# Kernel optimization log

Hardware: AMD Instinct MI355X
Metric: run time of the kernel (lower is better)

Reference implementation:

```python
import jax, jax.numpy as jnp
import numpy as np

DROPOUT_P = 0.5


def normalize_adj(A):
    # A_tilda = A + I ; A_hat = D^-0.5 A_tilda D^-0.5
    # The torch code does this with diag_embed + two bmm (O(N^3));
    # mathematically it is row/col broadcasting (O(N^2)).
    B, N, _ = A.shape
    A_tilda = A + jnp.eye(N, dtype=A.dtype)
    d_inv_sqrt = jnp.sum(A_tilda, axis=2) ** -0.5          # [B, N]
    return d_inv_sqrt[:, :, None] * A_tilda * d_inv_sqrt[:, None, :]


def gcn_layer(X, A_hat, W, b):
    # standard Kipf GCN layer: A_hat @ (X @ W) + b
    return jnp.einsum('bnm,bmd->bnd', A_hat, X @ W) + b


def setup_inputs() -> dict:
    key = jax.random.key(0)
    ks = jax.random.split(key, 6)
    B, N, Din, H, C = 8, 2048, 64, 64, 16
    X = jax.random.normal(ks[0], (B, N, Din), dtype=jnp.float32)
    A = jax.random.uniform(ks[1], (B, N, N), dtype=jnp.float32)
    W1 = jax.random.normal(ks[2], (Din, H), dtype=jnp.float32) * (1.0 / np.sqrt(Din))
    b1 = jax.random.normal(ks[3], (H,), dtype=jnp.float32) * 0.01
    W2 = jax.random.normal(ks[4], (H, C), dtype=jnp.float32) * (1.0 / np.sqrt(H))
    b2 = jax.random.normal(ks[5], (C,), dtype=jnp.float32) * 0.01
    return {"X": X, "A": A, "W1": W1, "b1": b1, "W2": W2, "b2": b2}


def reference(X, A, W1, b1, W2, b2):
    A_hat = normalize_adj(A)
    h = jax.nn.relu(gcn_layer(X, A_hat, W1, b1))
    # F.dropout default training=True -> apply dropout with a fixed key
    keep = jax.random.bernoulli(jax.random.key(42), 1.0 - DROPOUT_P, h.shape)
    h = jnp.where(keep, h / (1.0 - DROPOUT_P), 0.0).astype(h.dtype)
    return gcn_layer(h, A_hat, W2, b2)
```

## Files before the change

### kernel.cpp

```cpp
#include <hip/hip_runtime.h>

#define BN 16384
#define NN 2048
#define DD 64
#define CC 16

typedef short bf16x8 __attribute__((ext_vector_type(8)));
typedef float f32x4 __attribute__((ext_vector_type(4)));
typedef unsigned short u16x4 __attribute__((ext_vector_type(4)));

__device__ __forceinline__ f32x4 mfma16(bf16x8 a, bf16x8 b, f32x4 c) {
  return __builtin_amdgcn_mfma_f32_16x16x32_bf16(a, b, c, 0, 0, 0);
}
__device__ __forceinline__ unsigned short f2bf(float f) {
  unsigned u = __float_as_uint(f);
  return (unsigned short)((u + 0x7FFFu + ((u >> 16) & 1u)) >> 16);
}
__device__ __forceinline__ float bf2f(unsigned short h) {
  return __uint_as_float(((unsigned)h) << 16);
}

__device__ __forceinline__ unsigned tf_bits(unsigned i) {
  unsigned x0 = 0u;
  unsigned x1 = i;
  const unsigned k0 = 0u, k1 = 42u, k2 = 0x1BD11BDAu ^ 0u ^ 42u;
  x0 += k0; x1 += k1;
#define TFR(r) { x0 += x1; x1 = (x1 << (r)) | (x1 >> (32 - (r))); x1 ^= x0; }
  TFR(13) TFR(15) TFR(26) TFR(6)
  x0 += k1; x1 += k2 + 1u;
  TFR(17) TFR(29) TFR(16) TFR(24)
  x0 += k2; x1 += k0 + 2u;
  TFR(13) TFR(15) TFR(26) TFR(6)
  x0 += k0; x1 += k1 + 3u;
  TFR(17) TFR(29) TFR(16) TFR(24)
  x0 += k1; x1 += k2 + 4u;
  TFR(13) TFR(15) TFR(26) TFR(6)
  x0 += k2; x1 += k0 + 5u;
#undef TFR
  return x0 ^ x1;
}


__global__ __launch_bounds__(256) void k_deg(const float* __restrict__ A,
    float* __restrict__ dis, unsigned short* __restrict__ Abf)
{
  const int w = threadIdx.x >> 6, lane = threadIdx.x & 63;
  const size_t row = (size_t)blockIdx.x * 4 + w;
  const float4* Arow = (const float4*)(A + row * NN);
  unsigned short* Brow = Abf + row * NN;
  float s = 0.f;
#pragma unroll
  for (int it = 0; it < 8; ++it) {
    float4 v = Arow[lane + 64 * it];
    s += (v.x + v.y) + (v.z + v.w);
    u16x4 p = { f2bf(v.x), f2bf(v.y), f2bf(v.z), f2bf(v.w) };
    *(u16x4*)(Brow + lane * 4 + it * 256) = p;
  }
#pragma unroll
  for (int m = 32; m; m >>= 1) s += __shfl_xor(s, m, 64);
  if (lane == 0) dis[row] = 1.0f / sqrtf(s + 1.0f);
}

__global__ __launch_bounds__(256) void k_xw1(const float* __restrict__ X,
    const float* __restrict__ W1, const float* __restrict__ dis,
    unsigned short* __restrict__ Y1s, unsigned short* __restrict__ Y1sT)
{
  __shared__ float Xs[64 * 65];
  const int tid = threadIdx.x;
  const int r0 = blockIdx.x * 64;
  const int b = r0 >> 11, kr0 = r0 & (NN - 1);
#pragma unroll
  for (int it = 0; it < 16; ++it) {
    int idx = it * 256 + tid;
    Xs[(idx >> 6) * 65 + (idx & 63)] = X[(size_t)r0 * DD + idx];
  }
  __syncthreads();
  const int wq = __builtin_amdgcn_readfirstlane(tid >> 6);
  const int lane = tid & 63;
  const int row = r0 + lane;
  float acc[16];
#pragma unroll
  for (int c = 0; c < 16; ++c) acc[c] = 0.f;
  const float* Xr = Xs + lane * 65;
  const float* W1p = W1 + wq * 16;
#pragma unroll
  for (int k = 0; k < 64; ++k) {
    const float xv = Xr[k];
#pragma unroll
    for (int c = 0; c < 16; ++c) acc[c] += xv * W1p[k * DD + c];
  }
  const float dv = dis[row];
#pragma unroll
  for (int c = 0; c < 16; ++c) acc[c] *= dv;
#pragma unroll
  for (int q = 0; q < 4; ++q) {
    u16x4 p = { f2bf(acc[q*4]), f2bf(acc[q*4+1]), f2bf(acc[q*4+2]), f2bf(acc[q*4+3]) };
    *(u16x4*)(Y1s + (size_t)row * DD + wq * 16 + q * 4) = p;
  }
#pragma unroll
  for (int it = 0; it < 16; ++it)
    Y1sT[((size_t)b * DD + wq * 16 + it) * NN + kr0 + lane] = f2bf(acc[it]);
}

__global__ __launch_bounds__(256) void k_gemm1(const unsigned short* __restrict__ Abf,
    const unsigned short* __restrict__ Y1sT, float* __restrict__ Z1)
{
  const int Mb = blockIdx.x >> 2, ks = blockIdx.x & 3;
  const int w = __builtin_amdgcn_readfirstlane((int)threadIdx.x >> 6);
  const int lane = threadIdx.x & 63;
  const int m15 = lane & 15, quad = lane >> 4;
  const int b = Mb >> 4;
  const int k0 = ks * 512 + quad * 8;
  const unsigned short* Ap0 = Abf + ((size_t)Mb * 128 + w * 16 + m15) * NN + k0;
  const unsigned short* Ap1 = Ap0 + (size_t)64 * NN;
  const unsigned short* Bp  = Y1sT + ((size_t)b * DD + m15) * NN + k0;
  const f32x4 zero = 0.f;
  f32x4 acc[2][4];
#pragma unroll
  for (int m = 0; m < 2; ++m)
#pragma unroll
    for (int t = 0; t < 4; ++t) acc[m][t] = zero;
  bf16x8 a0 = *(const bf16x8*)Ap0;
  bf16x8 a1 = *(const bf16x8*)Ap1;
  bf16x8 b0 = *(const bf16x8*)(Bp);
  bf16x8 b1 = *(const bf16x8*)(Bp + 16 * NN);
  bf16x8 b2 = *(const bf16x8*)(Bp + 32 * NN);
  bf16x8 b3 = *(const bf16x8*)(Bp + 48 * NN);
  for (int kk = 0; kk < 16; ++kk) {
    const int off = (kk < 15) ? (kk + 1) * 32 : 0;
    bf16x8 na0 = *(const bf16x8*)(Ap0 + off);
    bf16x8 na1 = *(const bf16x8*)(Ap1 + off);
    bf16x8 nb0 = *(const bf16x8*)(Bp + off);
    bf16x8 nb1 = *(const bf16x8*)(Bp + 16 * NN + off);
    bf16x8 nb2 = *(const bf16x8*)(Bp + 32 * NN + off);
    bf16x8 nb3 = *(const bf16x8*)(Bp + 48 * NN + off);
    acc[0][0] = mfma16(a0, b0, acc[0][0]);
    acc[0][1] = mfma16(a0, b1, acc[0][1]);
    acc[0][2] = mfma16(a0, b2, acc[0][2]);
    acc[0][3] = mfma16(a0, b3, acc[0][3]);
    acc[1][0] = mfma16(a1, b0, acc[1][0]);
    acc[1][1] = mfma16(a1, b1, acc[1][1]);
    acc[1][2] = mfma16(a1, b2, acc[1][2]);
    acc[1][3] = mfma16(a1, b3, acc[1][3]);
    a0 = na0; a1 = na1; b0 = nb0; b1 = nb1; b2 = nb2; b3 = nb3;
  }
  const int rb0 = Mb * 128 + w * 16 + quad * 4;
#pragma unroll
  for (int m = 0; m < 2; ++m)
#pragma unroll
    for (int t = 0; t < 4; ++t)
#pragma unroll
      for (int r = 0; r < 4; ++r)
        Z1[((size_t)ks * BN + rb0 + m * 64 + r) * DD + t * 16 + m15] = acc[m][t][r];
}

__global__ __launch_bounds__(256) void k_epi1(const float* __restrict__ Z1,
    const unsigned short* __restrict__ Y1s, const float* __restrict__ dis,
    const float* __restrict__ b1, const float* __restrict__ W2,
    unsigned short* __restrict__ Y2sT)
{
  __shared__ float hs[64 * 65];
  __shared__ float W2l[DD * CC];
  const int tid = threadIdx.x;
  const int r0 = blockIdx.x * 64;
  const int b = r0 >> 11, kr0 = r0 & (NN - 1);
  *(float4*)(W2l + tid * 4) = *(const float4*)(W2 + tid * 4);
  const int n = tid & 63, wg = tid >> 6;
  const float bias = b1[n];
#pragma unroll
  for (int i = 0; i < 16; ++i) {
    const int rl = wg * 16 + i;
    const size_t row = (size_t)r0 + rl;
    const size_t o = row * DD + n;
    float z = bf2f(Y1s[o]);
#pragma unroll
    for (int p = 0; p < 4; ++p) z += Z1[((size_t)p * BN + row) * DD + n];
    float h = fmaxf(dis[row] * z + bias, 0.f);
    const unsigned bits = tf_bits((unsigned)o);
    h = (bits >> 31) ? 0.f : (h + h);
    hs[rl * 65 + n] = h;
  }
  __syncthreads();
  const int c = tid & 15, rg = tid >> 4;
  float y[4];
#pragma unroll
  for (int rr = 0; rr < 4; ++rr) {
    const int rl = rg * 4 + rr;
    float s = 0.f;
#pragma unroll
    for (int k = 0; k < 64; ++k) s += hs[rl * 65 + k] * W2l[k * CC + c];
    y[rr] = dis[r0 + rl] * s;
  }
  u16x4 pk = { f2bf(y[0]), f2bf(y[1]), f2bf(y[2]), f2bf(y[3]) };
  *(u16x4*)(Y2sT + ((size_t)b * CC + c) * NN + kr0 + rg * 4) = pk;
}

__global__ __launch_bounds__(256) void k_gemm2(const unsigned short* __restrict__ Abf,
    const unsigned short* __restrict__ Y2sT, float* __restrict__ Z2)
{
  const int Mb = blockIdx.x >> 3, ks = blockIdx.x & 7;
  const int w = __builtin_amdgcn_readfirstlane((int)threadIdx.x >> 6);
  const int lane = threadIdx.x & 63;
  const int m15 = lane & 15, quad = lane >> 4;
  const int b = Mb >> 3;
  const int k0 = ks * 256 + quad * 8;
  const unsigned short* Ap = Abf + ((size_t)Mb * 256 + w * 16 + m15) * NN + k0;
  const unsigned short* Bp = Y2sT + ((size_t)b * CC + m15) * NN + k0;
  const f32x4 zero = 0.f;
  f32x4 acc[4];
#pragma unroll
  for (int m = 0; m < 4; ++m) acc[m] = zero;
  bf16x8 a[4];
#pragma unroll
  for (int m = 0; m < 4; ++m) a[m] = *(const bf16x8*)(Ap + (size_t)m * 64 * NN);
  bf16x8 bb = *(const bf16x8*)Bp;
  for (int kk = 0; kk < 8; ++kk) {
    const int off = (kk < 7) ? (kk + 1) * 32 : 0;
    bf16x8 na[4];
#pragma unroll
    for (int m = 0; m < 4; ++m) na[m] = *(const bf16x8*)(Ap + (size_t)m * 64 * NN + off);
    bf16x8 nbb = *(const bf16x8*)(Bp + off);
#pragma unroll
    for (int m = 0; m < 4; ++m) acc[m] = mfma16(a[m], bb, acc[m]);
#pragma unroll
    for (int m = 0; m < 4; ++m) a[m] = na[m];
    bb = nbb;
  }
  const int rb0 = Mb * 256 + w * 16 + quad * 4;
#pragma unroll
  for (int m = 0; m < 4; ++m)
#pragma unroll
    for (int r = 0; r < 4; ++r)
      Z2[((size_t)ks * BN + rb0 + m * 64 + r) * CC + m15] = acc[m][r];
}

__global__ __launch_bounds__(256) void k_final(const float* __restrict__ Z2,
    const unsigned short* __restrict__ Y2sT, const float* __restrict__ dis,
    const float* __restrict__ b2, float* __restrict__ out)
{
  const int r = blockIdx.x * 256 + threadIdx.x;
  const int b = r >> 11, kr = r & (NN - 1);
  float s[16];
#pragma unroll
  for (int c = 0; c < 16; ++c) s[c] = bf2f(Y2sT[((size_t)b * CC + c) * NN + kr]);
#pragma unroll
  for (int p = 0; p < 8; ++p)
#pragma unroll
    for (int q = 0; q < 4; ++q) {
      float4 v = *(const float4*)(Z2 + ((size_t)p * BN + r) * CC + q * 4);
      s[q*4+0] += v.x; s[q*4+1] += v.y; s[q*4+2] += v.z; s[q*4+3] += v.w;
    }
  const float dv = dis[r];
#pragma unroll
  for (int q = 0; q < 4; ++q) {
    float4 o4;
    o4.x = dv * s[q*4+0] + b2[q*4+0];
    o4.y = dv * s[q*4+1] + b2[q*4+1];
    o4.z = dv * s[q*4+2] + b2[q*4+2];
    o4.w = dv * s[q*4+3] + b2[q*4+3];
    *(float4*)(out + (size_t)r * CC + q * 4) = o4;
  }
}

#define FKS1 4
#define FKS2 16

__global__ __launch_bounds__(256) void d_deg_xw(const float* __restrict__ A,
    const float* __restrict__ X, const float* __restrict__ W1,
    float* __restrict__ dis, float* __restrict__ Y1s)
{
  const int w = threadIdx.x >> 6, lane = threadIdx.x & 63;
  const int row = __builtin_amdgcn_readfirstlane(blockIdx.x * 4 + w);
  const float4* Arow = (const float4*)(A + (size_t)row * NN);
  float s = 0.f;
#pragma unroll
  for (int it = 0; it < 8; ++it) {
    float4 v = Arow[lane + 64 * it];
    s += v.x + v.y + v.z + v.w;
  }
#pragma unroll
  for (int m = 32; m; m >>= 1) s += __shfl_xor(s, m, 64);
  const float dv = 1.0f / sqrtf(s + 1.0f);
  if (lane == 0) dis[row] = dv;
  const float* Xr = X + (size_t)row * DD;
  float acc = 0.f;
#pragma unroll
  for (int k = 0; k < DD; ++k) acc += Xr[k] * W1[k * DD + lane];
  Y1s[(size_t)row * DD + lane] = dv * acc;
}

__global__ __launch_bounds__(256) void d_gemm1(const float* __restrict__ A,
    const float* __restrict__ Y1s, float* __restrict__ Z1)
{
  const int rb = blockIdx.x >> 2, ks = blockIdx.x & (FKS1 - 1);
  const int lane = threadIdx.x & 63;
  const int c0 = __builtin_amdgcn_readfirstlane((threadIdx.x >> 6) << 4);
  const int row = rb * 64 + lane;
  const int batch = rb >> 5;
  const int KSEG = NN / FKS1;
  const float* Arow = A + (size_t)row * NN + ks * KSEG;
  const float* Yb = Y1s + (size_t)batch * NN * DD + c0;
  const int kbase = ks * KSEG;
  float acc[16];
#pragma unroll
  for (int c = 0; c < 16; ++c) acc[c] = 0.f;
  float4 a0 = *(const float4*)(Arow);
  float4 a1 = *(const float4*)(Arow + 4);
  float4 a2 = *(const float4*)(Arow + 8);
  float4 a3 = *(const float4*)(Arow + 12);
  for (int k = 0; k < KSEG; k += 16) {
    const int kn = (k + 16 < KSEG) ? (k + 16) : 0;
    float4 n0 = *(const float4*)(Arow + kn);
    float4 n1 = *(const float4*)(Arow + kn + 4);
    float4 n2 = *(const float4*)(Arow + kn + 8);
    float4 n3 = *(const float4*)(Arow + kn + 12);
    const float* y0 = Yb + (size_t)(kbase + k) * DD;
    const float av[16] = {a0.x, a0.y, a0.z, a0.w, a1.x, a1.y, a1.z, a1.w,
                          a2.x, a2.y, a2.z, a2.w, a3.x, a3.y, a3.z, a3.w};
#pragma unroll
    for (int j = 0; j < 16; ++j) {
      const float* yr = y0 + j * DD;
#pragma unroll
      for (int c = 0; c < 16; ++c) acc[c] += av[j] * yr[c];
    }
    a0 = n0; a1 = n1; a2 = n2; a3 = n3;
  }
  float* Zp = Z1 + ((size_t)ks * BN + row) * DD + c0;
#pragma unroll
  for (int c = 0; c < 16; c += 4) {
    float4 v; v.x = acc[c]; v.y = acc[c+1]; v.z = acc[c+2]; v.w = acc[c+3];
    *(float4*)(Zp + c) = v;
  }
}

__global__ __launch_bounds__(256) void d_epi1(const float* __restrict__ Z1,
    const float* __restrict__ Y1s, const float* __restrict__ dis,
    const float* __restrict__ b1, const float* __restrict__ W2,
    float* __restrict__ Y2s)
{
  __shared__ float W2l[DD * CC];
  __shared__ float hl[4][DD];
  const int tid = threadIdx.x;
  *(float4*)(W2l + tid * 4) = *(const float4*)(W2 + tid * 4);
  const int w = tid >> 6, lane = tid & 63;
  const int row = blockIdx.x * 4 + w;
  const size_t o = (size_t)row * DD + lane;
  float z = Y1s[o];
#pragma unroll
  for (int p = 0; p < FKS1; ++p) z += Z1[(size_t)p * BN * DD + o];
  const float dv = dis[row];
  float h = fmaxf(dv * z + b1[lane], 0.f);
  const unsigned bits = tf_bits((unsigned)o);
  h = (bits >> 31) ? 0.f : (h + h);
  hl[w][lane] = h;
  __syncthreads();
  const int wr = tid >> 6, l = tid & 63;
  const int c = l & 15, kq = l >> 4;
  float p = 0.f;
#pragma unroll
  for (int kk = 0; kk < 16; ++kk)
    p += hl[wr][kq * 16 + kk] * W2l[(kq * 16 + kk) * CC + c];
  p += __shfl_xor(p, 16, 64);
  p += __shfl_xor(p, 32, 64);
  if (l < 16) {
    const int rg = blockIdx.x * 4 + wr;
    Y2s[(size_t)rg * CC + c] = dis[rg] * p;
  }
}

__global__ __launch_bounds__(256) void d_gemm2(const float* __restrict__ A,
    const float* __restrict__ Y2s, float* __restrict__ Z2)
{
  const int rb = blockIdx.x >> 4, ks = blockIdx.x & (FKS2 - 1);
  const int row = rb * 256 + threadIdx.x;
  const int batch = rb >> 3;
  const int KSEG = NN / FKS2;
  const float* Arow = A + (size_t)row * NN + ks * KSEG;
  const float* Yb = Y2s + (size_t)batch * NN * CC;
  const int kbase = ks * KSEG;
  float acc[16];
#pragma unroll
  for (int c = 0; c < 16; ++c) acc[c] = 0.f;
  float4 a0 = *(const float4*)(Arow);
  float4 a1 = *(const float4*)(Arow + 4);
  for (int k = 0; k < KSEG; k += 8) {
    const int kn = (k + 8 < KSEG) ? (k + 8) : 0;
    float4 n0 = *(const float4*)(Arow + kn);
    float4 n1 = *(const float4*)(Arow + kn + 4);
    const float av[8] = {a0.x, a0.y, a0.z, a0.w, a1.x, a1.y, a1.z, a1.w};
#pragma unroll
    for (int j = 0; j < 8; ++j) {
      const float* yr = Yb + (size_t)(kbase + k + j) * CC;
#pragma unroll
      for (int c = 0; c < 16; ++c) acc[c] += av[j] * yr[c];
    }
    a0 = n0; a1 = n1;
  }
  float* Zp = Z2 + ((size_t)ks * BN + row) * CC;
#pragma unroll
  for (int c = 0; c < 16; c += 4) {
    float4 v; v.x = acc[c]; v.y = acc[c+1]; v.z = acc[c+2]; v.w = acc[c+3];
    *(float4*)(Zp + c) = v;
  }
}

__global__ __launch_bounds__(256) void d_final(const float* __restrict__ Z2,
    const float* __restrict__ Y2s, const float* __restrict__ dis,
    const float* __restrict__ b2, float* __restrict__ out)
{
  const int gid = blockIdx.x * 256 + threadIdx.x;
  const int r = gid >> 2, q = gid & 3;
  const size_t o = (size_t)r * CC + q * 4;
  float4 s = *(const float4*)(Y2s + o);
#pragma unroll
  for (int p = 0; p < FKS2; ++p) {
    const float4 zp = *(const float4*)(Z2 + (size_t)p * BN * CC + o);
    s.x += zp.x; s.y += zp.y; s.z += zp.z; s.w += zp.w;
  }
  const float dv = dis[r];
  const float4 bb = *(const float4*)(b2 + q * 4);
  float4 res;
  res.x = dv * s.x + bb.x;
  res.y = dv * s.y + bb.y;
  res.z = dv * s.z + bb.z;
  res.w = dv * s.w + bb.w;
  *(float4*)(out + o) = res;
}

extern "C" void kernel_launch(void* const* d_in, const int* in_sizes, int n_in,
                              void* d_out, int out_size, void* d_ws, size_t ws_size,
                              hipStream_t stream) {
  const float* X  = (const float*)d_in[0];
  const float* A  = (const float*)d_in[1];
  const float* W1 = (const float*)d_in[2];
  const float* b1 = (const float*)d_in[3];
  const float* W2 = (const float*)d_in[4];
  const float* b2 = (const float*)d_in[5];
  float* out = (float*)d_out;
  char* wsb = (char*)d_ws;

  const size_t NEED = 88670208;
  if (ws_size >= NEED) {
    unsigned short* Abf  = (unsigned short*)wsb;
    float*          Z1   = (float*)(wsb + 67108864);
    float*          Z2   = Z1;
    float*          dis  = (float*)(wsb + 83886080);
    unsigned short* Y1s  = (unsigned short*)(wsb + 83951616);
    unsigned short* Y1sT = (unsigned short*)(wsb + 86048768);
    unsigned short* Y2sT = (unsigned short*)(wsb + 88145920);

    k_deg  <<<BN / 4, 256, 0, stream>>>(A, dis, Abf);
    k_xw1  <<<BN / 64, 256, 0, stream>>>(X, W1, dis, Y1s, Y1sT);
    k_gemm1<<<512,    256, 0, stream>>>(Abf, Y1sT, Z1);
    k_epi1 <<<BN / 64, 256, 0, stream>>>(Z1, Y1s, dis, b1, W2, Y2sT);
    k_gemm2<<<512,    256, 0, stream>>>(Abf, Y2sT, Z2);
    k_final<<<BN / 256, 256, 0, stream>>>(Z2, Y2sT, dis, b2, out);
  } else {
    float* ws  = (float*)d_ws;
    float* dis = ws;
    float* Y1s = ws + 16384;
    float* Z1  = Y1s + (size_t)BN * DD;
    float* Z2  = Z1;
    float* Y2s = Z1 + (size_t)FKS1 * BN * DD;

    d_deg_xw<<<BN / 4,     256, 0, stream>>>(A, X, W1, dis, Y1s);
    d_gemm1 <<<256 * FKS1, 256, 0, stream>>>(A, Y1s, Z1);
    d_epi1  <<<BN / 4,     256, 0, stream>>>(Z1, Y1s, dis, b1, W2, Y2s);
    d_gemm2 <<<64 * FKS2,  256, 0, stream>>>(A, Y2s, Z2);
    d_final <<<256,        256, 0, stream>>>(Z2, Y2s, dis, b2, out);
  }
}
```

Baseline: 277.5 us.

## Increase split-K in both aggregation GEMMs and use MFMA for X@W1

Both aggregation GEMMs now launch 1024 blocks instead of 512. GEMM1 is split 8-way along K and 2-way along the output columns, with 256-row tiles. GEMM2 is split 16-way along K. The epilogue kernels add up the larger number of partial sums, and the workspace grows to hold them. The X@W1 kernel now uses bf16 MFMA in place of the scalar FP32 shared-memory loop. The goal is more parallelism and occupancy on a mostly memory-bound pass over A. The cost is extra partial-sum traffic, rereading A in GEMM1 for the two column halves, and lower precision in X@W1.

Result: no change. 278.0 us (+0.2%).

```diff
diff --git a/kernel.cpp b/kernel.cpp
--- a/kernel.cpp
+++ b/kernel.cpp
@@ -4,6 +4,8 @@
 #define NN 2048
 #define DD 64
 #define CC 16
+#define KS1 8
+#define KS2 16
 
 typedef short bf16x8 __attribute__((ext_vector_type(8)));
 typedef float f32x4 __attribute__((ext_vector_type(4)));
@@ -65,93 +67,94 @@
     const float* __restrict__ W1, const float* __restrict__ dis,
     unsigned short* __restrict__ Y1s, unsigned short* __restrict__ Y1sT)
 {
-  __shared__ float Xs[64 * 65];
   const int tid = threadIdx.x;
+  const int w = __builtin_amdgcn_readfirstlane(tid >> 6);
+  const int lane = tid & 63;
+  const int m15 = lane & 15, quad = lane >> 4;
   const int r0 = blockIdx.x * 64;
   const int b = r0 >> 11, kr0 = r0 & (NN - 1);
-#pragma unroll
-  for (int it = 0; it < 16; ++it) {
-    int idx = it * 256 + tid;
-    Xs[(idx >> 6) * 65 + (idx & 63)] = X[(size_t)r0 * DD + idx];
-  }
-  __syncthreads();
-  const int wq = __builtin_amdgcn_readfirstlane(tid >> 6);
-  const int lane = tid & 63;
-  const int row = r0 + lane;
-  float acc[16];
-#pragma unroll
-  for (int c = 0; c < 16; ++c) acc[c] = 0.f;
-  const float* Xr = Xs + lane * 65;
-  const float* W1p = W1 + wq * 16;
-#pragma unroll
-  for (int k = 0; k < 64; ++k) {
-    const float xv = Xr[k];
-#pragma unroll
-    for (int c = 0; c < 16; ++c) acc[c] += xv * W1p[k * DD + c];
-  }
-  const float dv = dis[row];
-#pragma unroll
-  for (int c = 0; c < 16; ++c) acc[c] *= dv;
-#pragma unroll
-  for (int q = 0; q < 4; ++q) {
-    u16x4 p = { f2bf(acc[q*4]), f2bf(acc[q*4+1]), f2bf(acc[q*4+2]), f2bf(acc[q*4+3]) };
-    *(u16x4*)(Y1s + (size_t)row * DD + wq * 16 + q * 4) = p;
-  }
-#pragma unroll
-  for (int it = 0; it < 16; ++it)
-    Y1sT[((size_t)b * DD + wq * 16 + it) * NN + kr0 + lane] = f2bf(acc[it]);
-}
-
-__global__ __launch_bounds__(256) void k_gemm1(const unsigned short* __restrict__ Abf,
+  const int arow = r0 + w * 16 + m15;
+  const f32x4 zero = 0.f;
+  f32x4 acc[4];
+#pragma unroll
+  for (int t = 0; t < 4; ++t) acc[t] = zero;
+#pragma unroll
+  for (int ksx = 0; ksx < 2; ++ksx) {
+    const float* xp = X + (size_t)arow * DD + ksx * 32 + quad * 8;
+    float4 x0 = *(const float4*)xp;
+    float4 x1 = *(const float4*)(xp + 4);
+    bf16x8 af = { (short)f2bf(x0.x), (short)f2bf(x0.y), (short)f2bf(x0.z), (short)f2bf(x0.w),
+                  (short)f2bf(x1.x), (short)f2bf(x1.y), (short)f2bf(x1.z), (short)f2bf(x1.w) };
+#pragma unroll
+    for (int t = 0; t < 4; ++t) {
+      const float* wp = W1 + (size_t)(ksx * 32 + quad * 8) * DD + t * 16 + m15;
+      bf16x8 bfr = { (short)f2bf(wp[0*DD]), (short)f2bf(wp[1*DD]), (short)f2bf(wp[2*DD]), (short)f2bf(wp[3*DD]),
+                     (short)f2bf(wp[4*DD]), (short)f2bf(wp[5*DD]), (short)f2bf(wp[6*DD]), (short)f2bf(wp[7*DD]) };
+      acc[t] = mfma16(af, bfr, acc[t]);
+    }
+  }
+#pragma unroll
+  for (int t = 0; t < 4; ++t)
+#pragma unroll
+    for (int r = 0; r < 4; ++r) {
+      const int rowo = r0 + w * 16 + quad * 4 + r;
+      const unsigned short v = f2bf(dis[rowo] * acc[t][r]);
+      Y1s[(size_t)rowo * DD + t * 16 + m15] = v;
+      Y1sT[((size_t)b * DD + t * 16 + m15) * NN + (kr0 + w * 16 + quad * 4 + r)] = v;
+    }
+}
+
+__global__ __launch_bounds__(256, 4) void k_gemm1(const unsigned short* __restrict__ Abf,
     const unsigned short* __restrict__ Y1sT, float* __restrict__ Z1)
 {
-  const int Mb = blockIdx.x >> 2, ks = blockIdx.x & 3;
+  const int Mb = blockIdx.x >> 4;
+  const int ns = (blockIdx.x >> 3) & 1;
+  const int ks = blockIdx.x & 7;
   const int w = __builtin_amdgcn_readfirstlane((int)threadIdx.x >> 6);
   const int lane = threadIdx.x & 63;
   const int m15 = lane & 15, quad = lane >> 4;
-  const int b = Mb >> 4;
-  const int k0 = ks * 512 + quad * 8;
-  const unsigned short* Ap0 = Abf + ((size_t)Mb * 128 + w * 16 + m15) * NN + k0;
-  const unsigned short* Ap1 = Ap0 + (size_t)64 * NN;
-  const unsigned short* Bp  = Y1sT + ((size_t)b * DD + m15) * NN + k0;
+  const int b = Mb >> 3;
+  const int k0 = ks * 256 + quad * 8;
+  const unsigned short* Ap[4];
+#pragma unroll
+  for (int m = 0; m < 4; ++m)
+    Ap[m] = Abf + ((size_t)Mb * 256 + m * 64 + w * 16 + m15) * NN + k0;
+  const unsigned short* Bp0 = Y1sT + ((size_t)b * DD + ns * 32 + m15) * NN + k0;
+  const unsigned short* Bp1 = Bp0 + (size_t)16 * NN;
   const f32x4 zero = 0.f;
-  f32x4 acc[2][4];
-#pragma unroll
-  for (int m = 0; m < 2; ++m)
-#pragma unroll
-    for (int t = 0; t < 4; ++t) acc[m][t] = zero;
-  bf16x8 a0 = *(const bf16x8*)Ap0;
-  bf16x8 a1 = *(const bf16x8*)Ap1;
-  bf16x8 b0 = *(const bf16x8*)(Bp);
-  bf16x8 b1 = *(const bf16x8*)(Bp + 16 * NN);
-  bf16x8 b2 = *(const bf16x8*)(Bp + 32 * NN);
-  bf16x8 b3 = *(const bf16x8*)(Bp + 48 * NN);
-  for (int kk = 0; kk < 16; ++kk) {
-    const int off = (kk < 15) ? (kk + 1) * 32 : 0;
-    bf16x8 na0 = *(const bf16x8*)(Ap0 + off);
-    bf16x8 na1 = *(const bf16x8*)(Ap1 + off);
-    bf16x8 nb0 = *(const bf16x8*)(Bp + off);
-    bf16x8 nb1 = *(const bf16x8*)(Bp + 16 * NN + off);
-    bf16x8 nb2 = *(const bf16x8*)(Bp + 32 * NN + off);
-    bf16x8 nb3 = *(const bf16x8*)(Bp + 48 * NN + off);
-    acc[0][0] = mfma16(a0, b0, acc[0][0]);
-    acc[0][1] = mfma16(a0, b1, acc[0][1]);
-    acc[0][2] = mfma16(a0, b2, acc[0][2]);
-    acc[0][3] = mfma16(a0, b3, acc[0][3]);
-    acc[1][0] = mfma16(a1, b0, acc[1][0]);
-    acc[1][1] = mfma16(a1, b1, acc[1][1]);
-    acc[1][2] = mfma16(a1, b2, acc[1][2]);
-    acc[1][3] = mfma16(a1, b3, acc[1][3]);
-    a0 = na0; a1 = na1; b0 = nb0; b1 = nb1; b2 = nb2; b3 = nb3;
-  }
-  const int rb0 = Mb * 128 + w * 16 + quad * 4;
-#pragma unroll
-  for (int m = 0; m < 2; ++m)
-#pragma unroll
-    for (int t = 0; t < 4; ++t)
+  f32x4 acc[4][2];
+#pragma unroll
+  for (int m = 0; m < 4; ++m) { acc[m][0] = zero; acc[m][1] = zero; }
+  bf16x8 a[4], b0, b1;
+#pragma unroll
+  for (int m = 0; m < 4; ++m) a[m] = *(const bf16x8*)Ap[m];
+  b0 = *(const bf16x8*)Bp0;
+  b1 = *(const bf16x8*)Bp1;
+#pragma unroll 1
+  for (int kk = 0; kk < 8; ++kk) {
+    const int off = (kk < 7) ? (kk + 1) * 32 : 0;
+    bf16x8 na[4], nb0, nb1;
+#pragma unroll
+    for (int m = 0; m < 4; ++m) na[m] = *(const bf16x8*)(Ap[m] + off);
+    nb0 = *(const bf16x8*)(Bp0 + off);
+    nb1 = *(const bf16x8*)(Bp1 + off);
+#pragma unroll
+    for (int m = 0; m < 4; ++m) {
+      acc[m][0] = mfma16(a[m], b0, acc[m][0]);
+      acc[m][1] = mfma16(a[m], b1, acc[m][1]);
+    }
+#pragma unroll
+    for (int m = 0; m < 4; ++m) a[m] = na[m];
+    b0 = nb0; b1 = nb1;
+  }
+#pragma unroll
+  for (int m = 0; m < 4; ++m)
+#pragma unroll
+    for (int t = 0; t < 2; ++t)
 #pragma unroll
       for (int r = 0; r < 4; ++r)
-        Z1[((size_t)ks * BN + rb0 + m * 64 + r) * DD + t * 16 + m15] = acc[m][t][r];
+        Z1[((size_t)ks * BN + Mb * 256 + m * 64 + w * 16 + quad * 4 + r) * DD
+           + ns * 32 + t * 16 + m15] = acc[m][t][r];
 }
 
 __global__ __launch_bounds__(256) void k_epi1(const float* __restrict__ Z1,
@@ -174,7 +177,7 @@
     const size_t o = row * DD + n;
     float z = bf2f(Y1s[o]);
 #pragma unroll
-    for (int p = 0; p < 4; ++p) z += Z1[((size_t)p * BN + row) * DD + n];
+    for (int p = 0; p < KS1; ++p) z += Z1[((size_t)p * BN + row) * DD + n];
     float h = fmaxf(dis[row] * z + bias, 0.f);
     const unsigned bits = tf_bits((unsigned)o);
     h = (bits >> 31) ? 0.f : (h + h);
@@ -195,43 +198,47 @@
   *(u16x4*)(Y2sT + ((size_t)b * CC + c) * NN + kr0 + rg * 4) = pk;
 }
 
-__global__ __launch_bounds__(256) void k_gemm2(const unsigned short* __restrict__ Abf,
+__global__ __launch_bounds__(256, 4) void k_gemm2(const unsigned short* __restrict__ Abf,
     const unsigned short* __restrict__ Y2sT, float* __restrict__ Z2)
 {
-  const int Mb = blockIdx.x >> 3, ks = blockIdx.x & 7;
+  const int Mb = blockIdx.x >> 4;
+  const int ks = blockIdx.x & 15;
   const int w = __builtin_amdgcn_readfirstlane((int)threadIdx.x >> 6);
   const int lane = threadIdx.x & 63;
   const int m15 = lane & 15, quad = lane >> 4;
   const int b = Mb >> 3;
-  const int k0 = ks * 256 + quad * 8;
-  const unsigned short* Ap = Abf + ((size_t)Mb * 256 + w * 16 + m15) * NN + k0;
+  const int k0 = ks * 128 + quad * 8;
+  const unsigned short* Ap[4];
+#pragma unroll
+  for (int m = 0; m < 4; ++m)
+    Ap[m] = Abf + ((size_t)Mb * 256 + m * 64 + w * 16 + m15) * NN + k0;
   const unsigned short* Bp = Y2sT + ((size_t)b * CC + m15) * NN + k0;
   const f32x4 zero = 0.f;
   f32x4 acc[4];
 #pragma unroll
   for (int m = 0; m < 4; ++m) acc[m] = zero;
-  bf16x8 a[4];
-#pragma unroll
-  for (int m = 0; m < 4; ++m) a[m] = *(const bf16x8*)(Ap + (size_t)m * 64 * NN);
-  bf16x8 bb = *(const bf16x8*)Bp;
-  for (int kk = 0; kk < 8; ++kk) {
-    const int off = (kk < 7) ? (kk + 1) * 32 : 0;
-    bf16x8 na[4];
-#pragma unroll
-    for (int m = 0; m < 4; ++m) na[m] = *(const bf16x8*)(Ap + (size_t)m * 64 * NN + off);
-    bf16x8 nbb = *(const bf16x8*)(Bp + off);
+  bf16x8 a[4], bb;
+#pragma unroll
+  for (int m = 0; m < 4; ++m) a[m] = *(const bf16x8*)Ap[m];
+  bb = *(const bf16x8*)Bp;
+#pragma unroll 1
+  for (int kk = 0; kk < 4; ++kk) {
+    const int off = (kk < 3) ? (kk + 1) * 32 : 0;
+    bf16x8 na[4], nbb;
+#pragma unroll
+    for (int m = 0; m < 4; ++m) na[m] = *(const bf16x8*)(Ap[m] + off);
+    nbb = *(const bf16x8*)(Bp + off);
 #pragma unroll
     for (int m = 0; m < 4; ++m) acc[m] = mfma16(a[m], bb, acc[m]);
 #pragma unroll
     for (int m = 0; m < 4; ++m) a[m] = na[m];
     bb = nbb;
   }
-  const int rb0 = Mb * 256 + w * 16 + quad * 4;
 #pragma unroll
   for (int m = 0; m < 4; ++m)
 #pragma unroll
     for (int r = 0; r < 4; ++r)
-      Z2[((size_t)ks * BN + rb0 + m * 64 + r) * CC + m15] = acc[m][r];
+      Z2[((size_t)ks * BN + Mb * 256 + m * 64 + w * 16 + quad * 4 + r) * CC + m15] = acc[m][r];
 }
 
 __global__ __launch_bounds__(256) void k_final(const float* __restrict__ Z2,
@@ -244,7 +251,7 @@
 #pragma unroll
   for (int c = 0; c < 16; ++c) s[c] = bf2f(Y2sT[((size_t)b * CC + c) * NN + kr]);
 #pragma unroll
-  for (int p = 0; p < 8; ++p)
+  for (int p = 0; p < KS2; ++p)
 #pragma unroll
     for (int q = 0; q < 4; ++q) {
       float4 v = *(const float4*)(Z2 + ((size_t)p * BN + r) * CC + q * 4);
@@ -439,21 +446,21 @@
   float* out = (float*)d_out;
   char* wsb = (char*)d_ws;
 
-  const size_t NEED = 88670208;
+  const size_t NEED = 105447424;
   if (ws_size >= NEED) {
     unsigned short* Abf  = (unsigned short*)wsb;
     float*          Z1   = (float*)(wsb + 67108864);
     float*          Z2   = Z1;
-    float*          dis  = (float*)(wsb + 83886080);
-    unsigned short* Y1s  = (unsigned short*)(wsb + 83951616);
-    unsigned short* Y1sT = (unsigned short*)(wsb + 86048768);
-    unsigned short* Y2sT = (unsigned short*)(wsb + 88145920);
-
-    k_deg  <<<BN / 4, 256, 0, stream>>>(A, dis, Abf);
+    float*          dis  = (float*)(wsb + 100663296);
+    unsigned short* Y1s  = (unsigned short*)(wsb + 100728832);
+    unsigned short* Y1sT = (unsigned short*)(wsb + 102825984);
+    unsigned short* Y2sT = (unsigned short*)(wsb + 104923136);
+
+    k_deg  <<<BN / 4,  256, 0, stream>>>(A, dis, Abf);
     k_xw1  <<<BN / 64, 256, 0, stream>>>(X, W1, dis, Y1s, Y1sT);
-    k_gemm1<<<512,    256, 0, stream>>>(Abf, Y1sT, Z1);
+    k_gemm1<<<1024,    256, 0, stream>>>(Abf, Y1sT, Z1);
     k_epi1 <<<BN / 64, 256, 0, stream>>>(Z1, Y1s, dis, b1, W2, Y2sT);
-    k_gemm2<<<512,    256, 0, stream>>>(Abf, Y2sT, Z2);
+    k_gemm2<<<1024,    256, 0, stream>>>(Abf, Y2sT, Z2);
     k_final<<<BN / 256, 256, 0, stream>>>(Z2, Y2sT, dis, b2, out);
   } else {
     float* ws  = (float*)d_ws;
```
